# Performance work log

Hardware: AMD Instinct MI355X
Metric: run time of the kernel (lower is better)

The kernel has to match this reference:

```python
import jax, jax.numpy as jnp
import numpy as np

B, C, H, W = 4, 5, 96, 96


def setup_inputs() -> dict:
    key = jax.random.key(0)
    ks = jax.random.split(key, 5)
    x = jax.random.normal(ks[0], (B, C, H, W), dtype=jnp.float32)
    wq = jax.random.normal(ks[1], (C, C), dtype=jnp.float32) * 0.1  # 1x1 conv weight [out,in]
    bq = jax.random.normal(ks[2], (C,), dtype=jnp.float32) * 0.1
    wk = jax.random.normal(ks[3], (C, C), dtype=jnp.float32) * 0.1
    bk = jax.random.normal(ks[4], (C,), dtype=jnp.float32) * 0.1
    return {"x": x, "wq": wq, "bq": bq, "wk": wk, "bk": bk}


def reference(x, wq, bq, wk, bk):
    b, c, h, w = x.shape
    n = h * w
    # 1x1 convs == per-pixel linear maps over channels
    q = jnp.einsum('bchw,oc->bohw', x, wq) + bq[None, :, None, None]
    k = jnp.einsum('bchw,oc->bohw', x, wk) + bk[None, :, None, None]
    proj_query = q.reshape(b, c, n).transpose(0, 2, 1)  # [B, N, C]
    proj_key = k.reshape(b, c, n)                        # [B, C, N]
    energy = jnp.einsum('bnc,bcm->bnm', proj_query, proj_key)  # [B, N, N], no scaling
    attention = jax.nn.softmax(energy, axis=-1)
    return attention
```

## Files before the change

kernel.cpp:

```cpp
#include <hip/hip_runtime.h>

constexpr int B_ = 4, C_ = 5, H_ = 96, W_ = 96;
constexpr int N_ = H_ * W_;
constexpr int NPT = N_ / 256;
constexpr int NJ = NPT / 4;

typedef float    f32x4 __attribute__((ext_vector_type(4)));
typedef _Float16 f16x4 __attribute__((ext_vector_type(4)));

__global__ __launch_bounds__(256) void proj_qk(
    const float* __restrict__ x,
    const float* __restrict__ wq, const float* __restrict__ bq,
    const float* __restrict__ wk, const float* __restrict__ bk,
    float* __restrict__ q, _Float16* __restrict__ k)
{
    int idx = blockIdx.x * 256 + threadIdx.x;
    if (idx >= B_ * N_) return;
    int b = idx / N_;
    int n = idx - b * N_;
    float xi[C_];
#pragma unroll
    for (int i = 0; i < C_; ++i) xi[i] = x[(size_t)(b * C_ + i) * N_ + n];
#pragma unroll
    for (int c = 0; c < C_; ++c) {
        float aq = bq[c], ak = bk[c];
#pragma unroll
        for (int i = 0; i < C_; ++i) {
            aq = fmaf(wq[c * C_ + i], xi[i], aq);
            ak = fmaf(wk[c * C_ + i], xi[i], ak);
        }
        q[(size_t)(b * C_ + c) * N_ + n] = aq;
        k[(size_t)(b * C_ + c) * N_ + n] = (_Float16)ak;
    }
}

__global__ __launch_bounds__(256) void attn_row(
    const float* __restrict__ q, const _Float16* __restrict__ k,
    float* __restrict__ out)
{
    const int row = blockIdx.x;
    const int b = row / N_;
    const int n = row - b * N_;
    const int tid = threadIdx.x;

    float qv[C_];
#pragma unroll
    for (int c = 0; c < C_; ++c) qv[c] = q[(size_t)(b * C_ + c) * N_ + n];

    const _Float16* kb = k + (size_t)b * C_ * N_;

    f32x4 e[NJ];
    float lmax = -3.4e38f;
#pragma unroll
    for (int j = 0; j < NJ; ++j) {
        const int m4 = (j * 256 + tid) * 4;
        f32x4 acc = {0.f, 0.f, 0.f, 0.f};
#pragma unroll
        for (int c = 0; c < C_; ++c) {
            const f16x4 kh = *reinterpret_cast<const f16x4*>(kb + (size_t)c * N_ + m4);
            acc.x = fmaf(qv[c], (float)kh.x, acc.x);
            acc.y = fmaf(qv[c], (float)kh.y, acc.y);
            acc.z = fmaf(qv[c], (float)kh.z, acc.z);
            acc.w = fmaf(qv[c], (float)kh.w, acc.w);
        }
        e[j] = acc;
        lmax = fmaxf(lmax, fmaxf(fmaxf(acc.x, acc.y), fmaxf(acc.z, acc.w)));
    }

    __shared__ float redmax[4];
    __shared__ float redsum[4];

#pragma unroll
    for (int off = 32; off >= 1; off >>= 1)
        lmax = fmaxf(lmax, __shfl_xor(lmax, off, 64));
    const int wv = tid >> 6;
    if ((tid & 63) == 0) redmax[wv] = lmax;
    __syncthreads();
    const float rmax = fmaxf(fmaxf(redmax[0], redmax[1]),
                             fmaxf(redmax[2], redmax[3]));

    float lsum = 0.f;
#pragma unroll
    for (int j = 0; j < NJ; ++j) {
        e[j].x = __expf(e[j].x - rmax);
        e[j].y = __expf(e[j].y - rmax);
        e[j].z = __expf(e[j].z - rmax);
        e[j].w = __expf(e[j].w - rmax);
        lsum += (e[j].x + e[j].y) + (e[j].z + e[j].w);
    }
#pragma unroll
    for (int off = 32; off >= 1; off >>= 1)
        lsum += __shfl_xor(lsum, off, 64);
    if ((tid & 63) == 0) redsum[wv] = lsum;
    __syncthreads();
    const float inv = 1.f / ((redsum[0] + redsum[1]) + (redsum[2] + redsum[3]));

    float* orow = out + (size_t)row * N_;
#pragma unroll
    for (int j = 0; j < NJ; ++j) {
        const int m4 = (j * 256 + tid) * 4;
        f32x4 o;
        o.x = e[j].x * inv;
        o.y = e[j].y * inv;
        o.z = e[j].z * inv;
        o.w = e[j].w * inv;
        *reinterpret_cast<f32x4*>(orow + m4) = o;
    }
}

extern "C" void kernel_launch(void* const* d_in, const int* in_sizes, int n_in,
                              void* d_out, int out_size, void* d_ws, size_t ws_size,
                              hipStream_t stream)
{
    const float* x  = (const float*)d_in[0];
    const float* wq = (const float*)d_in[1];
    const float* bq = (const float*)d_in[2];
    const float* wk = (const float*)d_in[3];
    const float* bk = (const float*)d_in[4];
    float* out = (float*)d_out;

    float*    q = (float*)d_ws;
    _Float16* k = (_Float16*)(q + (size_t)B_ * C_ * N_);

    proj_qk<<<(B_ * N_ + 255) / 256, 256, 0, stream>>>(x, wq, bq, wk, bk, q, k);
    attn_row<<<B_ * N_, 256, 0, stream>>>(q, k, out);
}
```

Baseline: 282.0 us.

## Process eight attention rows per block, keeping K slice in registers

Each block now handles eight consecutive query rows instead of one, loading the block's K columns into registers once and reusing them across rows. This cuts repeated K reads from global/L2 and block launch overhead. In exchange it adds register pressure (kr holds 5x9 f16x4 per thread plus e[9]) under a launch bound of 3 blocks per CU, and the grid has fewer blocks. The kernel is dominated by writing the 4x9216x9216 fp32 output, so the gain may be limited.

Result: slower. 799.3 us (+183.4%).

```diff
diff --git a/kernel.cpp b/kernel.cpp
--- a/kernel.cpp
+++ b/kernel.cpp
@@ -4,6 +4,7 @@
 constexpr int N_ = H_ * W_;
 constexpr int NPT = N_ / 256;
 constexpr int NJ = NPT / 4;
+constexpr int ROWS = 8;
 
 typedef float    f32x4 __attribute__((ext_vector_type(4)));
 typedef _Float16 f16x4 __attribute__((ext_vector_type(4)));
@@ -34,77 +35,89 @@
     }
 }
 
-__global__ __launch_bounds__(256) void attn_row(
+__global__ __launch_bounds__(256, 3) void attn_rows(
     const float* __restrict__ q, const _Float16* __restrict__ k,
     float* __restrict__ out)
 {
-    const int row = blockIdx.x;
-    const int b = row / N_;
-    const int n = row - b * N_;
+    constexpr int BPB = N_ / ROWS;
+    const int g  = blockIdx.x;
+    const int b  = g / BPB;
+    const int n0 = (g - b * BPB) * ROWS;
     const int tid = threadIdx.x;
-
-    float qv[C_];
-#pragma unroll
-    for (int c = 0; c < C_; ++c) qv[c] = q[(size_t)(b * C_ + c) * N_ + n];
+    const int wv  = tid >> 6;
 
     const _Float16* kb = k + (size_t)b * C_ * N_;
 
-    f32x4 e[NJ];
-    float lmax = -3.4e38f;
+    f16x4 kr[C_][NJ];
 #pragma unroll
-    for (int j = 0; j < NJ; ++j) {
-        const int m4 = (j * 256 + tid) * 4;
-        f32x4 acc = {0.f, 0.f, 0.f, 0.f};
+    for (int c = 0; c < C_; ++c)
 #pragma unroll
-        for (int c = 0; c < C_; ++c) {
-            const f16x4 kh = *reinterpret_cast<const f16x4*>(kb + (size_t)c * N_ + m4);
-            acc.x = fmaf(qv[c], (float)kh.x, acc.x);
-            acc.y = fmaf(qv[c], (float)kh.y, acc.y);
-            acc.z = fmaf(qv[c], (float)kh.z, acc.z);
-            acc.w = fmaf(qv[c], (float)kh.w, acc.w);
-        }
-        e[j] = acc;
-        lmax = fmaxf(lmax, fmaxf(fmaxf(acc.x, acc.y), fmaxf(acc.z, acc.w)));
-    }
+        for (int j = 0; j < NJ; ++j)
+            kr[c][j] = *reinterpret_cast<const f16x4*>(
+                kb + (size_t)c * N_ + (j * 256 + tid) * 4);
 
     __shared__ float redmax[4];
     __shared__ float redsum[4];
 
+    for (int r = 0; r < ROWS; ++r) {
+        const int n = n0 + r;
+
+        float qv[C_];
 #pragma unroll
-    for (int off = 32; off >= 1; off >>= 1)
-        lmax = fmaxf(lmax, __shfl_xor(lmax, off, 64));
-    const int wv = tid >> 6;
-    if ((tid & 63) == 0) redmax[wv] = lmax;
-    __syncthreads();
-    const float rmax = fmaxf(fmaxf(redmax[0], redmax[1]),
-                             fmaxf(redmax[2], redmax[3]));
+        for (int c = 0; c < C_; ++c)
+            qv[c] = q[(size_t)(b * C_ + c) * N_ + n];
 
-    float lsum = 0.f;
+        f32x4 e[NJ];
+        float lmax = -3.4e38f;
 #pragma unroll
-    for (int j = 0; j < NJ; ++j) {
-        e[j].x = __expf(e[j].x - rmax);
-        e[j].y = __expf(e[j].y - rmax);
-        e[j].z = __expf(e[j].z - rmax);
-        e[j].w = __expf(e[j].w - rmax);
-        lsum += (e[j].x + e[j].y) + (e[j].z + e[j].w);
-    }
+        for (int j = 0; j < NJ; ++j) {
+            f32x4 acc = {0.f, 0.f, 0.f, 0.f};
 #pragma unroll
-    for (int off = 32; off >= 1; off >>= 1)
-        lsum += __shfl_xor(lsum, off, 64);
-    if ((tid & 63) == 0) redsum[wv] = lsum;
-    __syncthreads();
-    const float inv = 1.f / ((redsum[0] + redsum[1]) + (redsum[2] + redsum[3]));
+            for (int c = 0; c < C_; ++c) {
+                acc.x = fmaf(qv[c], (float)kr[c][j].x, acc.x);
+                acc.y = fmaf(qv[c], (float)kr[c][j].y, acc.y);
+                acc.z = fmaf(qv[c], (float)kr[c][j].z, acc.z);
+                acc.w = fmaf(qv[c], (float)kr[c][j].w, acc.w);
+            }
+            e[j] = acc;
+            lmax = fmaxf(lmax, fmaxf(fmaxf(acc.x, acc.y), fmaxf(acc.z, acc.w)));
+        }
 
-    float* orow = out + (size_t)row * N_;
 #pragma unroll
-    for (int j = 0; j < NJ; ++j) {
-        const int m4 = (j * 256 + tid) * 4;
-        f32x4 o;
-        o.x = e[j].x * inv;
-        o.y = e[j].y * inv;
-        o.z = e[j].z * inv;
-        o.w = e[j].w * inv;
-        *reinterpret_cast<f32x4*>(orow + m4) = o;
+        for (int off = 32; off >= 1; off >>= 1)
+            lmax = fmaxf(lmax, __shfl_xor(lmax, off, 64));
+        if ((tid & 63) == 0) redmax[wv] = lmax;
+        __syncthreads();
+        const float rmax = fmaxf(fmaxf(redmax[0], redmax[1]),
+                                 fmaxf(redmax[2], redmax[3]));
+
+        float lsum = 0.f;
+#pragma unroll
+        for (int j = 0; j < NJ; ++j) {
+            e[j].x = __expf(e[j].x - rmax);
+            e[j].y = __expf(e[j].y - rmax);
+            e[j].z = __expf(e[j].z - rmax);
+            e[j].w = __expf(e[j].w - rmax);
+            lsum += (e[j].x + e[j].y) + (e[j].z + e[j].w);
+        }
+#pragma unroll
+        for (int off = 32; off >= 1; off >>= 1)
+            lsum += __shfl_xor(lsum, off, 64);
+        if ((tid & 63) == 0) redsum[wv] = lsum;
+        __syncthreads();
+        const float inv = 1.f / ((redsum[0] + redsum[1]) +
+                                 (redsum[2] + redsum[3]));
+
+        float* orow = out + (size_t)(b * N_ + n) * N_;
+#pragma unroll
+        for (int j = 0; j < NJ; ++j) {
+            f32x4 o;
+            o.x = e[j].x * inv;
+            o.y = e[j].y * inv;
+            o.z = e[j].z * inv;
+            o.w = e[j].w * inv;
+            *reinterpret_cast<f32x4*>(orow + (j * 256 + tid) * 4) = o;
+        }
     }
 }
 
@@ -123,5 +136,5 @@
     _Float16* k = (_Float16*)(q + (size_t)B_ * C_ * N_);
 
     proj_qk<<<(B_ * N_ + 255) / 256, 256, 0, stream>>>(x, wq, bq, wk, bk, q, k);
-    attn_row<<<B_ * N_, 256, 0, stream>>>(q, k, out);
+    attn_rows<<<B_ * (N_ / ROWS), 256, 0, stream>>>(q, k, out);
 }
```
